# Optimization experiments

Hardware: AMD Instinct MI355X
Metric: run time of the kernel (lower is better)

The kernel has to match this reference:

```python
import jax, jax.numpy as jnp
import numpy as np

L = 16            # clip_len
STRIDES = (2, 2)
RADII = (0.15, 0.3)
NSAMPLES = (16, 32)
EPS = 1e-5
NEG_SLOPE = 0.2


def _fps(xyz, npoint):
    # furthest point sampling, xyz: (N, 3) -> (npoint,) int32 indices, start at 0
    N = xyz.shape[0]
    def step(carry, _):
        mind, last = carry
        d = jnp.sum((xyz - xyz[last]) ** 2, axis=-1)
        mind = jnp.minimum(mind, d)
        nxt = jnp.argmax(mind).astype(jnp.int32)
        return (mind, nxt), nxt
    _, rest = jax.lax.scan(step, (jnp.full((N,), 1e10, xyz.dtype), jnp.int32(0)), None, length=npoint - 1)
    return jnp.concatenate([jnp.zeros((1,), jnp.int32), rest])


def _shift_point(xyz, batch, N):
    # torch.roll(points, -1, dims=1) over the temporal axis, with last-frame extrapolation fix
    p = xyz.reshape(batch // L, L, N, 3)
    s = jnp.roll(p, -1, axis=1)
    shift_mean = jnp.mean(s[:, :-1] - p[:, :-1], axis=1)   # (Bc, N, 3)
    s = s.at[:, -1].set(p[:, -1] + shift_mean)
    return s.reshape(batch, N, 3)


def _conv_bn_lrelu(x, w, g, b):
    # 1x1 Conv2d (no bias) + GroupBN (per-channel over all other dims) + LeakyReLU(0.2)
    y = jnp.einsum('oc,bcnk->bonk', w, x)
    mu = jnp.mean(y, axis=(0, 2, 3), keepdims=True)
    var = jnp.var(y, axis=(0, 2, 3), keepdims=True)
    y = (y - mu) * jax.lax.rsqrt(var + EPS) * g[None, :, None, None] + b[None, :, None, None]
    return jnp.where(y > 0, y, NEG_SLOPE * y)


def _sa_module(xyz, features, stride, radius, nsample, layers):
    # xyz: (B, N, 3), features: (B, C, N)
    batch, N = xyz.shape[0], xyz.shape[1]
    q = _shift_point(xyz, batch, N)
    npoint = N // stride if stride > 1 else N
    if stride > 1:
        idx = jax.vmap(lambda p: _fps(p, npoint))(jax.lax.stop_gradient(q))  # (B, npoint)
        q = jax.vmap(lambda p, ix: p[ix])(q, idx)                            # (B, npoint, 3)
    # ball query: first `nsample` neighbors of each query within `radius`, padded with first hit
    d2 = jnp.sum((q[:, :, None, :] - xyz[:, None, :, :]) ** 2, axis=-1)      # (B, npoint, N)
    mask = d2 < radius * radius
    cand = jnp.where(mask, jnp.arange(N, dtype=jnp.int32)[None, None, :], N)
    srt = jnp.sort(cand, axis=-1)[..., :nsample]
    first = srt[..., :1]
    gidx = jnp.where(srt == N, first, srt)
    gidx = jnp.where(gidx == N, 0, gidx)                                     # fallback: no neighbor
    grouped_xyz = jax.vmap(lambda pts, ix: pts[ix])(xyz, gidx)               # (B, npoint, ns, 3)
    dp = (grouped_xyz - q[:, :, None, :]) / radius                           # normalize_dp
    dist = jnp.linalg.norm(dp, axis=-1)                                      # (B, npoint, ns) -> 4th grouped channel
    feats = jnp.swapaxes(features, 1, 2)                                     # (B, N, C)
    grouped_f = jax.vmap(lambda f, ix: f[ix])(feats, gidx)                   # (B, npoint, ns, C)
    x = jnp.concatenate([dp, grouped_f], axis=-1)                            # (B, npoint, ns, 3 + C)
    x = jnp.transpose(x, (0, 3, 1, 2))                                       # (B, 3 + C, npoint, ns)
    for (w, g, b) in layers:
        x = _conv_bn_lrelu(x, w, g, b)
    gate = jax.nn.sigmoid(dist)[:, None, :, :]                               # sigmoid(points[:, -1:])
    out = jnp.max(gate * x, axis=-1)                                         # (B, Cout, npoint)
    return q, out


def _forward(xyz, w1a, g1a, b1a, w1b, g1b, b1b, w2a, g2a, b2a, w2b, g2b, b2b):
    features = jnp.swapaxes(xyz, 1, 2)                                       # features default = xyz^T
    q1, f1 = _sa_module(xyz, features, STRIDES[0], RADII[0], NSAMPLES[0],
                        [(w1a, g1a, b1a), (w1b, g1b, b1b)])
    q2, f2 = _sa_module(q1, f1, STRIDES[1], RADII[1], NSAMPLES[1],
                        [(w2a, g2a, b2a), (w2b, g2b, b2b)])
    return f2                                                                # (32, 256, 128)


def setup_inputs() -> dict:
    key = jax.random.key(0)
    ks = jax.random.split(key, 5)
    B, N = 32, 512   # B = 2 clips * clip_len 16
    xyz = jax.random.uniform(ks[0], (B, N, 3), jnp.float32)
    def w(k, o, i):
        return jax.random.normal(k, (o, i), jnp.float32) / np.sqrt(i).astype(np.float32)
    return {
        'xyz': xyz,
        'w1a': w(ks[1], 64, 6),    'g1a': jnp.ones(64),  'b1a': jnp.zeros(64),
        'w1b': w(ks[2], 128, 64),  'g1b': jnp.ones(128), 'b1b': jnp.zeros(128),
        'w2a': w(ks[3], 128, 131), 'g2a': jnp.ones(128), 'b2a': jnp.zeros(128),
        'w2b': w(ks[4], 256, 128), 'g2b': jnp.ones(256), 'b2b': jnp.zeros(256),
    }


def reference(xyz, w1a, g1a, b1a, w1b, g1b, b1b, w2a, g2a, b2a, w2b, g2b, b2b):
    return _forward(xyz, w1a, g1a, b1a, w1b, g1b, b1b, w2a, g2a, b2a, w2b, g2b, b2b)
```

## Files before the change

kernel.cpp:

```cpp
#include <hip/hip_runtime.h>
#include <hip/hip_bf16.h>
#include <math.h>


#define BATCH 32
#define MCOLS 131072
#define CGRID 2048

typedef __attribute__((ext_vector_type(8))) short short8;
typedef __attribute__((ext_vector_type(4))) short short4v;
typedef __attribute__((ext_vector_type(4))) float f32x4;

__device__ __forceinline__ float b2f(short s) {
    return __uint_as_float(((unsigned)(unsigned short)s) << 16);
}
__device__ __forceinline__ short f2b(float f) {
    __hip_bfloat16 h = __float2bfloat16(f);
    return (short)__builtin_bit_cast(unsigned short, h);
}
__device__ __forceinline__ float dpp_row16_sum(float v) {
    int x;
    x = __builtin_amdgcn_update_dpp(0, __float_as_int(v), 0x111, 0xf, 0xf, true);
    v += __int_as_float(x);
    x = __builtin_amdgcn_update_dpp(0, __float_as_int(v), 0x112, 0xf, 0xf, true);
    v += __int_as_float(x);
    x = __builtin_amdgcn_update_dpp(0, __float_as_int(v), 0x114, 0xf, 0xf, true);
    v += __int_as_float(x);
    x = __builtin_amdgcn_update_dpp(0, __float_as_int(v), 0x118, 0xf, 0xf, true);
    v += __int_as_float(x);
    return v;
}
template<int C>
__device__ __forceinline__ float dpp_max(float v) {
    int x = __builtin_amdgcn_update_dpp(0, __float_as_int(v), C, 0xf, 0xf, true);
    return fmaxf(v, __int_as_float(x));
}
__device__ __forceinline__ float readlane_f(float v, int lane) {
    return __int_as_float(__builtin_amdgcn_readlane(__float_as_int(v), lane));
}

__global__ void prep_w(const float* __restrict__ w, int O, int C, int CK,
                       short* __restrict__ hi, short* __restrict__ lo) {
    int t = blockIdx.x * 256 + threadIdx.x;
    if (t >= O * CK) return;
    int o = t / CK, c = t % CK;
    float f = (c < C) ? w[o * C + c] : 0.f;
    short h = f2b(f);
    float fh = b2f(h);
    int NT = O >> 4;
    int ot = o >> 4, l15 = o & 15;
    int kc = c >> 5, quad = (c & 31) >> 3, j = c & 7;
    size_t idx = (((size_t)kc * NT + ot) * 64 + quad * 16 + l15) * 8 + j;
    hi[idx] = h;
    lo[idx] = f2b(f - fh);
}

template<int N, int NPOINT>
__global__ __launch_bounds__(64) void fps_kernel(const float* __restrict__ src,
                                                 float* __restrict__ qsel) {
    int b = blockIdx.x;
    int lane = threadIdx.x;
    int l = b & 15;
    constexpr int P = N / 64;
    __shared__ float4 qp[N];
    __shared__ int sel[NPOINT];
    if (l < 15) {
        const float* s = src + (size_t)(b + 1) * N * 3;
        for (int j = lane; j < N; j += 64)
            qp[j] = make_float4(s[j * 3 + 0], s[j * 3 + 1], s[j * 3 + 2], 0.f);
    } else {
        int g0 = b - 15;
        for (int j = lane; j < N; j += 64) {
            float v[3];
#pragma unroll
            for (int c = 0; c < 3; ++c) {
                float acc = 0.f;
                for (int i = 0; i < 15; ++i) {
                    float d = __fsub_rn(src[((size_t)(g0 + i + 1) * N + j) * 3 + c],
                                        src[((size_t)(g0 + i) * N + j) * 3 + c]);
                    acc = __fadd_rn(acc, d);
                }
                v[c] = __fadd_rn(src[((size_t)b * N + j) * 3 + c], __fdiv_rn(acc, 15.f));
            }
            qp[j] = make_float4(v[0], v[1], v[2], 0.f);
        }
    }
    if (lane == 0) sel[0] = 0;
    __syncthreads();
    float px[P], py[P], pz[P], mind[P];
#pragma unroll
    for (int p = 0; p < P; ++p) {
        float4 v = qp[lane * P + p];
        px[p] = v.x; py[p] = v.y; pz[p] = v.z;
        mind[p] = 1e10f;
    }
    float4 L0 = qp[0];
    float lx = L0.x, ly = L0.y, lz = L0.z;
    for (int s = 1; s < NPOINT; ++s) {
        float mn[P];
#pragma unroll
        for (int p = 0; p < P; ++p) {
            float dx = __fsub_rn(px[p], lx);
            float dy = __fsub_rn(py[p], ly);
            float dz = __fsub_rn(pz[p], lz);
            float d = __fadd_rn(__fadd_rn(__fmul_rn(dx, dx), __fmul_rn(dy, dy)),
                                __fmul_rn(dz, dz));
            float m2 = fminf(mind[p], d);
            mind[p] = m2;
            mn[p] = m2;
        }
        float t[P];
#pragma unroll
        for (int p = 0; p < P; ++p) t[p] = mn[p];
#pragma unroll
        for (int w = P / 2; w >= 1; w >>= 1)
#pragma unroll
            for (int p = 0; p < w; ++p) t[p] = fmaxf(t[p], t[p + w]);
        float local = t[0];
        float m = local;
        m = dpp_max<0x111>(m);
        m = dpp_max<0x112>(m);
        m = dpp_max<0x114>(m);
        m = dpp_max<0x118>(m);
        m = dpp_max<0x142>(m);
        m = dpp_max<0x143>(m);
        float maxd = readlane_f(m, 63);
        int enc = 0;
        float bx = px[0], by = py[0], bz = pz[0];
#pragma unroll
        for (int p = P - 1; p >= 1; --p) {
            bool e = (mn[p] == local);
            enc = e ? p : enc;
            bx = e ? px[p] : bx;
            by = e ? py[p] : by;
            bz = e ? pz[p] : bz;
        }
        bool e0 = (mn[0] == local);
        enc = e0 ? 0 : enc;
        bx = e0 ? px[0] : bx;
        by = e0 ? py[0] : by;
        bz = e0 ? pz[0] : bz;
        unsigned long long msk = __ballot(local == maxd);
        int winner = (int)__builtin_ctzll(msk);
        int last = winner * P + __builtin_amdgcn_readlane(enc, winner);
        lx = readlane_f(bx, winner);
        ly = readlane_f(by, winner);
        lz = readlane_f(bz, winner);
        if (lane == 0) sel[s] = last;
    }
    __syncthreads();
    for (int i = lane; i < NPOINT; i += 64) {
        float4 Pt = qp[sel[i]];
        size_t o = ((size_t)b * NPOINT + i) * 3;
        qsel[o + 0] = Pt.x;
        qsel[o + 1] = Pt.y;
        qsel[o + 2] = Pt.z;
    }
}

template<int N, int NPOINT, int NS, int CF, int CK>
__global__ __launch_bounds__(256) void ballq_kernel(
        const float* __restrict__ xyz,
        const float* __restrict__ qpts,
        const float* __restrict__ feats,
        float r2, float radius,
        short* __restrict__ X, float* __restrict__ gate) {
    static_assert((NS & (NS - 1)) == 0, "NS pow2");
    int lane = threadIdx.x & 63;
    int wib = threadIdx.x >> 6;
    int wid = blockIdx.x * 4 + wib;
    int b = wid / NPOINT;
    int i = wid % NPOINT;
    const float* qp = qpts + ((size_t)b * NPOINT + i) * 3;
    float qx = qp[0], qy = qp[1], qz = qp[2];
    __shared__ int gsh[4][NS];
    int* gidx = gsh[wib];
    int taken = 0, first = 0;
    bool any = false;
#pragma unroll
    for (int base = 0; base < N; base += 64) {
        int j = base + lane;
        const float* p = xyz + ((size_t)b * N + j) * 3;
        float dx = __fsub_rn(qx, p[0]);
        float dy = __fsub_rn(qy, p[1]);
        float dz = __fsub_rn(qz, p[2]);
        float d2 = __fadd_rn(__fadd_rn(__fmul_rn(dx, dx), __fmul_rn(dy, dy)),
                             __fmul_rn(dz, dz));
        bool in = d2 < r2;
        unsigned long long mk = __ballot(in);
        if (!any && mk) { first = base + __builtin_ctzll(mk); any = true; }
        int cb = __builtin_popcountll(mk & ((1ull << lane) - 1ull));
        int slot = taken + cb;
        if (in && slot < NS) gidx[slot] = j;
        taken += (int)__builtin_popcountll(mk);
    }
    if (taken < NS) {
        for (int s = taken + lane; s < NS; s += 64) gidx[s] = any ? first : 0;
    }
    __syncthreads();
    int m0 = (b * NPOINT + i) * NS;
    if (lane < NS) {
        int g = gidx[lane];
        const float* p = xyz + ((size_t)b * N + g) * 3;
        float dx = (p[0] - qx) / radius;
        float dy = (p[1] - qy) / radius;
        float dz = (p[2] - qz) / radius;
        float dist = sqrtf(dx * dx + dy * dy + dz * dz);
        gate[m0 + lane] = 1.f / (1.f + expf(-dist));
    }
    for (int e = lane; e < NS * CK; e += 64) {
        int s = e / CK;
        int c = e % CK;
        int g = gidx[s];
        float v;
        if (c < 3) {
            float qc = (c == 0) ? qx : ((c == 1) ? qy : qz);
            v = (xyz[((size_t)b * N + g) * 3 + c] - qc) / radius;
        } else if (c < 3 + CF) {
            v = feats[((size_t)b * N + g) * CF + (c - 3)];
        } else {
            v = 0.f;
        }
        X[(size_t)(m0 + s) * CK + c] = f2b(v);
    }
}

template<int CK, int O, bool AFF>
__global__ __launch_bounds__(256, 3) void mfma_conv(
        const short* __restrict__ X, const short* __restrict__ Whi,
        const short* __restrict__ Wlo, const float* __restrict__ ss,
        short* __restrict__ Y, float* __restrict__ pS, float* __restrict__ pS2) {
    constexpr int KC = CK / 32;
    constexpr int NT = O / 16;
    constexpr int OW = NT / 4;
    constexpr int LR = CK + 8;
    constexpr int CB = CK / 8;
    __shared__ __align__(16) short xs[64 * LR];
    __shared__ __align__(16) short wh[NT * 512];
    __shared__ __align__(16) short wl[NT * 512];
    __shared__ float ssl[AFF ? 2 * CK : 1];
    __shared__ float sblk[O], s2blk[O];
    int tid = threadIdx.x;
    int m0 = blockIdx.x * 64;

    if constexpr (AFF) {
        for (int i = tid; i < 2 * CK; i += 256) ssl[i] = ss[i];
        __syncthreads();
    }
    for (int idx = tid; idx < 64 * CB; idx += 256) {
        int r = idx / CB;
        int col = (idx % CB) * 8;
        short8 v = *(const short8*)(X + (size_t)(m0 + r) * CK + col);
        if constexpr (AFF) {
#pragma unroll
            for (int i = 0; i < 8; ++i) {
                float f = b2f(v[i]);
                f = fmaf(f, ssl[col + i], ssl[CK + col + i]);
                f = f > 0.f ? f : 0.2f * f;
                v[i] = f2b(f);
            }
        }
        *(short8*)(xs + r * LR + col) = v;
    }

    int lane = tid & 63;
    int wave = tid >> 6;
    int l15 = lane & 15;
    int quad = lane >> 4;
    int obase = wave * OW * 16;

    f32x4 acc[4][OW];
#pragma unroll
    for (int mt = 0; mt < 4; ++mt)
#pragma unroll
        for (int ot = 0; ot < OW; ++ot) acc[mt][ot] = (f32x4){0.f, 0.f, 0.f, 0.f};

    for (int kc = 0; kc < KC; ++kc) {
        __syncthreads();
        {
            const short8* gH = (const short8*)Whi + (size_t)kc * NT * 64;
            const short8* gL = (const short8*)Wlo + (size_t)kc * NT * 64;
            short8* lH = (short8*)wh;
            short8* lL = (short8*)wl;
            for (int i = tid; i < NT * 64; i += 256) { lH[i] = gH[i]; lL[i] = gL[i]; }
        }
        __syncthreads();
        short8 bf[4];
#pragma unroll
        for (int mt = 0; mt < 4; ++mt)
            bf[mt] = *(const short8*)(xs + (mt * 16 + l15) * LR + kc * 32 + quad * 8);
#pragma unroll
        for (int ot = 0; ot < OW; ++ot) {
            short8 ah = ((const short8*)wh)[(wave * OW + ot) * 64 + lane];
            short8 al = ((const short8*)wl)[(wave * OW + ot) * 64 + lane];
#pragma unroll
            for (int mt = 0; mt < 4; ++mt) {
                acc[mt][ot] = __builtin_amdgcn_mfma_f32_16x16x32_bf16(ah, bf[mt], acc[mt][ot], 0, 0, 0);
                acc[mt][ot] = __builtin_amdgcn_mfma_f32_16x16x32_bf16(al, bf[mt], acc[mt][ot], 0, 0, 0);
            }
        }
    }

#pragma unroll
    for (int mt = 0; mt < 4; ++mt) {
        size_t ybase = (size_t)(m0 + mt * 16 + l15) * O + obase + quad * 4;
#pragma unroll
        for (int ot = 0; ot < OW; ++ot) {
            short4v pk;
#pragma unroll
            for (int r4 = 0; r4 < 4; ++r4) pk[r4] = f2b(acc[mt][ot][r4]);
            *(short4v*)(Y + ybase + ot * 16) = pk;
        }
    }
#pragma unroll
    for (int ot = 0; ot < OW; ++ot) {
#pragma unroll
        for (int r4 = 0; r4 < 4; ++r4) {
            float s = 0.f, s2 = 0.f;
#pragma unroll
            for (int mt = 0; mt < 4; ++mt) {
                float v = acc[mt][ot][r4];
                s += v;
                s2 = fmaf(v, v, s2);
            }
            s = dpp_row16_sum(s);
            s2 = dpp_row16_sum(s2);
            if (l15 == 15) {
                int o = obase + ot * 16 + quad * 4 + r4;
                sblk[o] = s;
                s2blk[o] = s2;
            }
        }
    }
    __syncthreads();
    for (int o = tid; o < O; o += 256) {
        pS [(size_t)o * CGRID + blockIdx.x] = sblk[o];
        pS2[(size_t)o * CGRID + blockIdx.x] = s2blk[o];
    }
}

template<int O>
__global__ __launch_bounds__(256) void stats_fin(
        const float* __restrict__ pS, const float* __restrict__ pS2,
        const float* __restrict__ gm, const float* __restrict__ bt,
        float* __restrict__ norm) {
    int o = blockIdx.x;
    float s = 0.f, s2 = 0.f;
    for (int p = threadIdx.x; p < CGRID; p += 256) {
        s += pS[(size_t)o * CGRID + p];
        s2 += pS2[(size_t)o * CGRID + p];
    }
#pragma unroll
    for (int off = 32; off >= 1; off >>= 1) {
        s  += __shfl_xor(s,  off, 64);
        s2 += __shfl_xor(s2, off, 64);
    }
    __shared__ float sh[8];
    int wid = threadIdx.x >> 6;
    if ((threadIdx.x & 63) == 0) { sh[wid] = s; sh[4 + wid] = s2; }
    __syncthreads();
    if (threadIdx.x == 0) {
        float S  = sh[0] + sh[1] + sh[2] + sh[3];
        float S2 = sh[4] + sh[5] + sh[6] + sh[7];
        const float invM = 1.f / (float)MCOLS;
        float mu = S * invM;
        float var = S2 * invM - mu * mu;
        float sc = gm[o] * rsqrtf(var + 1e-5f);
        norm[o] = sc;
        norm[O + o] = bt[o] - mu * sc;
    }
}

template<int NS, int NPOINT, int O>
__global__ __launch_bounds__(256) void pool1_kernel(
        const short* __restrict__ Y, const float* __restrict__ norm,
        const float* __restrict__ gate, float* __restrict__ out) {
    int t = blockIdx.x * 256 + threadIdx.x;
    int o = t % O;
    int n = (t / O) % NPOINT;
    int b = t / (O * NPOINT);
    int m0 = (b * NPOINT + n) * NS;
    float sc = norm[o], sf = norm[O + o];
    float best = -INFINITY;
#pragma unroll
    for (int k = 0; k < NS; ++k) {
        float v = fmaf(b2f(Y[(size_t)(m0 + k) * O + o]), sc, sf);
        v = v > 0.f ? v : 0.2f * v;
        best = fmaxf(best, gate[m0 + k] * v);
    }
    out[t] = best;
}

__global__ __launch_bounds__(256) void pool2_kernel(
        const short* __restrict__ Y, const float* __restrict__ norm,
        const float* __restrict__ gate, float* __restrict__ out) {
    constexpr int NS = 32, NPOINT = 128, O = 256;
    int b  = blockIdx.x >> 3;
    int oc = (blockIdx.x >> 1) & 3;
    int nc = blockIdx.x & 1;
    __shared__ float trans[64][65];
    int tid = threadIdx.x;
    for (int w = 0; w < 16; ++w) {
        int idx = w * 256 + tid;
        int o_l = idx & 63;
        int n_l = idx >> 6;
        int o = oc * 64 + o_l;
        int n = nc * 64 + n_l;
        int m0 = (b * NPOINT + n) * NS;
        float sc = norm[o], sf = norm[O + o];
        float best = -INFINITY;
#pragma unroll
        for (int k = 0; k < NS; ++k) {
            float v = fmaf(b2f(Y[(size_t)(m0 + k) * O + o]), sc, sf);
            v = v > 0.f ? v : 0.2f * v;
            best = fmaxf(best, gate[m0 + k] * v);
        }
        trans[o_l][n_l] = best;
    }
    __syncthreads();
    for (int w = 0; w < 16; ++w) {
        int idx = w * 256 + tid;
        int o_l = idx >> 6;
        int n_l = idx & 63;
        out[((size_t)b * O + oc * 64 + o_l) * NPOINT + nc * 64 + n_l] = trans[o_l][n_l];
    }
}

extern "C" void kernel_launch(void* const* d_in, const int* in_sizes, int n_in,
                              void* d_out, int out_size, void* d_ws, size_t ws_size,
                              hipStream_t stream) {
    const float* xyz = (const float*)d_in[0];
    const float* w1a = (const float*)d_in[1];
    const float* g1a = (const float*)d_in[2];
    const float* b1a = (const float*)d_in[3];
    const float* w1b = (const float*)d_in[4];
    const float* g1b = (const float*)d_in[5];
    const float* b1b = (const float*)d_in[6];
    const float* w2a = (const float*)d_in[7];
    const float* g2a = (const float*)d_in[8];
    const float* b2a = (const float*)d_in[9];
    const float* w2b = (const float*)d_in[10];
    const float* g2b = (const float*)d_in[11];
    const float* b2b = (const float*)d_in[12];

    char* ws = (char*)d_ws;
    constexpr size_t OFF_Q1C   = 0;
    constexpr size_t OFF_GATE1 = 98304;
    constexpr size_t OFF_Q2C   = 622592;
    constexpr size_t OFF_GATE2 = 671744;
    constexpr size_t OFF_NORM  = 1196032;
    constexpr size_t OFF_W     = 1204224;
    constexpr size_t OFF_PS    = 1499136;
    constexpr size_t OFF_PS2   = 3596288;
    constexpr size_t OFF_A     = 5693440;
    constexpr size_t OFF_B     = 39247872;
    constexpr size_t OFF_F1    = OFF_B + 41943040;

    float* q1c   = (float*)(ws + OFF_Q1C);
    float* gate1 = (float*)(ws + OFF_GATE1);
    float* q2c   = (float*)(ws + OFF_Q2C);
    float* gate2 = (float*)(ws + OFF_GATE2);
    float* n1a   = (float*)(ws + OFF_NORM);
    float* n1b   = (float*)(ws + OFF_NORM + 512);
    float* n2a   = (float*)(ws + OFF_NORM + 1536);
    float* n2b   = (float*)(ws + OFF_NORM + 2560);
    short* w1aH  = (short*)(ws + OFF_W);
    short* w1aL  = w1aH + 2048;
    short* w1bH  = w1aL + 2048;
    short* w1bL  = w1bH + 8192;
    short* w2aH  = w1bL + 8192;
    short* w2aL  = w2aH + 20480;
    short* w2bH  = w2aL + 20480;
    short* w2bL  = w2bH + 32768;
    float* pS    = (float*)(ws + OFF_PS);
    float* pS2   = (float*)(ws + OFF_PS2);

    char* A = ws + OFF_A;
    char* B = ws + OFF_B;
    short* X1  = (short*)A;
    short* Y1a = (short*)B;
    short* Y1b = (short*)A;
    short* X2  = (short*)B;
    short* Y2a = (short*)A;
    short* Y2b = (short*)B;
    float* f1  = (float*)(ws + OFF_F1);

    const float r2_1 = (float)(0.15 * 0.15);
    const float r2_2 = (float)(0.3 * 0.3);

    prep_w<<<8,   256, 0, stream>>>(w1a, 64, 6, 32, w1aH, w1aL);
    prep_w<<<32,  256, 0, stream>>>(w1b, 128, 64, 64, w1bH, w1bL);
    prep_w<<<80,  256, 0, stream>>>(w2a, 128, 131, 160, w2aH, w2aL);
    prep_w<<<128, 256, 0, stream>>>(w2b, 256, 128, 128, w2bH, w2bL);

    fps_kernel<512, 256><<<32, 64, 0, stream>>>(xyz, q1c);
    ballq_kernel<512, 256, 16, 3, 32><<<2048, 256, 0, stream>>>(
        xyz, q1c, xyz, r2_1, 0.15f, X1, gate1);
    mfma_conv<32, 64, false><<<CGRID, 256, 0, stream>>>(X1, w1aH, w1aL, nullptr, Y1a, pS, pS2);
    stats_fin<64><<<64, 256, 0, stream>>>(pS, pS2, g1a, b1a, n1a);
    mfma_conv<64, 128, true><<<CGRID, 256, 0, stream>>>(Y1a, w1bH, w1bL, n1a, Y1b, pS, pS2);
    stats_fin<128><<<128, 256, 0, stream>>>(pS, pS2, g1b, b1b, n1b);
    pool1_kernel<16, 256, 128><<<4096, 256, 0, stream>>>(Y1b, n1b, gate1, f1);

    fps_kernel<256, 128><<<32, 64, 0, stream>>>(q1c, q2c);
    ballq_kernel<256, 128, 32, 128, 160><<<1024, 256, 0, stream>>>(
        q1c, q2c, f1, r2_2, 0.3f, X2, gate2);
    mfma_conv<160, 128, false><<<CGRID, 256, 0, stream>>>(X2, w2aH, w2aL, nullptr, Y2a, pS, pS2);
    stats_fin<128><<<128, 256, 0, stream>>>(pS, pS2, g2a, b2a, n2a);
    mfma_conv<128, 256, true><<<CGRID, 256, 0, stream>>>(Y2a, w2bH, w2bL, n2a, Y2b, pS, pS2);
    stats_fin<256><<<256, 256, 0, stream>>>(pS, pS2, g2b, b2b, n2b);
    pool2_kernel<<<256, 256, 0, stream>>>(Y2b, n2b, gate2, (float*)d_out);
}
```

Baseline: 434.3 us.

## Fuse setup kernels, atomic BN stats, drop stats_fin, parallelize shift, vectorize stores

Merges the four weight-prep launches and the temporal shift into one setup kernel, moving the shift out of the serial FPS kernel into fully parallel per-element work. BatchNorm partial sums are now accumulated with atomics into a small zeroed buffer, and the scale/shift is recomputed inside consumer kernels, so the separate stats_fin launches go away. Conv outputs are staged through LDS for coalesced 16-byte stores, and ball-query gather writes eight bf16 values at once. Atomic float accumulation makes the statistics order-nondeterministic and adds contention on a few addresses.

```diff
diff --git a/kernel.cpp b/kernel.cpp
--- a/kernel.cpp
+++ b/kernel.cpp
@@ -39,9 +39,9 @@
     return __int_as_float(__builtin_amdgcn_readlane(__float_as_int(v), lane));
 }
 
-__global__ void prep_w(const float* __restrict__ w, int O, int C, int CK,
-                       short* __restrict__ hi, short* __restrict__ lo) {
-    int t = blockIdx.x * 256 + threadIdx.x;
+__device__ __forceinline__ void prep_elem(const float* __restrict__ w, int O, int C,
+                                          int CK, short* __restrict__ hi,
+                                          short* __restrict__ lo, int t) {
     if (t >= O * CK) return;
     int o = t / CK, c = t % CK;
     float f = (c < C) ? w[o * C + c] : 0.f;
@@ -55,36 +55,57 @@
     lo[idx] = f2b(f - fh);
 }
 
+__device__ __forceinline__ void shift_elem(const float* __restrict__ xyz,
+                                           float* __restrict__ qout, int t, int N) {
+    int c = t % 3;
+    int n = (t / 3) % N;
+    int b = t / (3 * N);
+    int l = b & 15;
+    float v;
+    if (l < 15) {
+        v = xyz[((size_t)(b + 1) * N + n) * 3 + c];
+    } else {
+        int g0 = b - 15;
+        float acc = 0.f;
+        for (int i = 0; i < 15; ++i) {
+            float d = __fsub_rn(xyz[((size_t)(g0 + i + 1) * N + n) * 3 + c],
+                                xyz[((size_t)(g0 + i) * N + n) * 3 + c]);
+            acc = __fadd_rn(acc, d);
+        }
+        v = __fadd_rn(xyz[((size_t)b * N + n) * 3 + c], __fdiv_rn(acc, 15.f));
+    }
+    qout[t] = v;
+}
+
+__global__ __launch_bounds__(256) void setup_kernel(
+        const float* __restrict__ w1a, const float* __restrict__ w1b,
+        const float* __restrict__ w2a, const float* __restrict__ w2b,
+        const float* __restrict__ xyz, float* __restrict__ qs1,
+        short* w1aH, short* w1aL, short* w1bH, short* w1bL,
+        short* w2aH, short* w2aL, short* w2bH, short* w2bL) {
+    int bid = blockIdx.x;
+    int tid = threadIdx.x;
+    if (bid < 8)        prep_elem(w1a, 64, 6, 32,    w1aH, w1aL, bid * 256 + tid);
+    else if (bid < 40)  prep_elem(w1b, 128, 64, 64,  w1bH, w1bL, (bid - 8) * 256 + tid);
+    else if (bid < 120) prep_elem(w2a, 128, 131, 160, w2aH, w2aL, (bid - 40) * 256 + tid);
+    else if (bid < 248) prep_elem(w2b, 256, 128, 128, w2bH, w2bL, (bid - 120) * 256 + tid);
+    else {
+        int t = (bid - 248) * 256 + tid;
+        if (t < BATCH * 512 * 3) shift_elem(xyz, qs1, t, 512);
+    }
+}
+
 template<int N, int NPOINT>
-__global__ __launch_bounds__(64) void fps_kernel(const float* __restrict__ src,
+__global__ __launch_bounds__(64) void fps_kernel(const float* __restrict__ q,
                                                  float* __restrict__ qsel) {
     int b = blockIdx.x;
     int lane = threadIdx.x;
-    int l = b & 15;
     constexpr int P = N / 64;
     __shared__ float4 qp[N];
     __shared__ int sel[NPOINT];
-    if (l < 15) {
-        const float* s = src + (size_t)(b + 1) * N * 3;
-        for (int j = lane; j < N; j += 64)
-            qp[j] = make_float4(s[j * 3 + 0], s[j * 3 + 1], s[j * 3 + 2], 0.f);
-    } else {
-        int g0 = b - 15;
-        for (int j = lane; j < N; j += 64) {
-            float v[3];
-#pragma unroll
-            for (int c = 0; c < 3; ++c) {
-                float acc = 0.f;
-                for (int i = 0; i < 15; ++i) {
-                    float d = __fsub_rn(src[((size_t)(g0 + i + 1) * N + j) * 3 + c],
-                                        src[((size_t)(g0 + i) * N + j) * 3 + c]);
-                    acc = __fadd_rn(acc, d);
-                }
-                v[c] = __fadd_rn(src[((size_t)b * N + j) * 3 + c], __fdiv_rn(acc, 15.f));
-            }
-            qp[j] = make_float4(v[0], v[1], v[2], 0.f);
-        }
-    }
+    const float* qb = q + (size_t)b * N * 3;
+    for (int j = lane; j < N; j += 64)
+        qp[j] = make_float4(qb[j * 3 + 0], qb[j * 3 + 1], qb[j * 3 + 2], 0.f);
     if (lane == 0) sel[0] = 0;
     __syncthreads();
     float px[P], py[P], pz[P], mind[P];
@@ -125,21 +146,16 @@
         m = dpp_max<0x142>(m);
         m = dpp_max<0x143>(m);
         float maxd = readlane_f(m, 63);
-        int enc = 0;
-        float bx = px[0], by = py[0], bz = pz[0];
-#pragma unroll
-        for (int p = P - 1; p >= 1; --p) {
+        int enc = P - 1;
+        float bx = px[P - 1], by = py[P - 1], bz = pz[P - 1];
+#pragma unroll
+        for (int p = P - 2; p >= 0; --p) {
             bool e = (mn[p] == local);
             enc = e ? p : enc;
             bx = e ? px[p] : bx;
             by = e ? py[p] : by;
             bz = e ? pz[p] : bz;
         }
-        bool e0 = (mn[0] == local);
-        enc = e0 ? 0 : enc;
-        bx = e0 ? px[0] : bx;
-        by = e0 ? py[0] : by;
-        bz = e0 ? pz[0] : bz;
         unsigned long long msk = __ballot(local == maxd);
         int winner = (int)__builtin_ctzll(msk);
         int last = winner * P + __builtin_amdgcn_readlane(enc, winner);
@@ -166,6 +182,7 @@
         float r2, float radius,
         short* __restrict__ X, float* __restrict__ gate) {
     static_assert((NS & (NS - 1)) == 0, "NS pow2");
+    static_assert(CK % 8 == 0, "CK mult of 8");
     int lane = threadIdx.x & 63;
     int wib = threadIdx.x >> 6;
     int wid = blockIdx.x * 4 + wib;
@@ -208,43 +225,64 @@
         float dist = sqrtf(dx * dx + dy * dy + dz * dz);
         gate[m0 + lane] = 1.f / (1.f + expf(-dist));
     }
-    for (int e = lane; e < NS * CK; e += 64) {
-        int s = e / CK;
-        int c = e % CK;
+    for (int e8 = lane * 8; e8 < NS * CK; e8 += 64 * 8) {
+        int s = e8 / CK;
+        int c0 = e8 % CK;
         int g = gidx[s];
-        float v;
-        if (c < 3) {
-            float qc = (c == 0) ? qx : ((c == 1) ? qy : qz);
-            v = (xyz[((size_t)b * N + g) * 3 + c] - qc) / radius;
-        } else if (c < 3 + CF) {
-            v = feats[((size_t)b * N + g) * CF + (c - 3)];
-        } else {
-            v = 0.f;
-        }
-        X[(size_t)(m0 + s) * CK + c] = f2b(v);
+        const float* frow = feats + (size_t)(b * N + g) * CF;
+        const float* prow = xyz + ((size_t)b * N + g) * 3;
+        short8 v8;
+#pragma unroll
+        for (int ii = 0; ii < 8; ++ii) {
+            int c = c0 + ii;
+            float v;
+            if (c < 3) {
+                float qc = (c == 0) ? qx : ((c == 1) ? qy : qz);
+                v = (prow[c] - qc) / radius;
+            } else if (c < 3 + CF) {
+                v = frow[c - 3];
+            } else {
+                v = 0.f;
+            }
+            v8[ii] = f2b(v);
+        }
+        *(short8*)(X + (size_t)(m0 + s) * CK + c0) = v8;
     }
 }
 
 template<int CK, int O, bool AFF>
 __global__ __launch_bounds__(256, 3) void mfma_conv(
         const short* __restrict__ X, const short* __restrict__ Whi,
-        const short* __restrict__ Wlo, const float* __restrict__ ss,
-        short* __restrict__ Y, float* __restrict__ pS, float* __restrict__ pS2) {
+        const short* __restrict__ Wlo,
+        const float* __restrict__ aS,
+        const float* __restrict__ gm, const float* __restrict__ bt,
+        float* __restrict__ mySums,
+        short* __restrict__ Y) {
     constexpr int KC = CK / 32;
     constexpr int NT = O / 16;
     constexpr int OW = NT / 4;
     constexpr int LR = CK + 8;
+    constexpr int LRY = O + 10;
     constexpr int CB = CK / 8;
-    __shared__ __align__(16) short xs[64 * LR];
+    constexpr int XSZ = (64 * LR > 32 * LRY) ? 64 * LR : 32 * LRY;
+    __shared__ __align__(16) short xsbuf[XSZ];
     __shared__ __align__(16) short wh[NT * 512];
     __shared__ __align__(16) short wl[NT * 512];
-    __shared__ float ssl[AFF ? 2 * CK : 1];
-    __shared__ float sblk[O], s2blk[O];
+    __shared__ float ssl[AFF ? 2 * CK : 2];
     int tid = threadIdx.x;
     int m0 = blockIdx.x * 64;
+    short* xs = xsbuf;
 
     if constexpr (AFF) {
-        for (int i = tid; i < 2 * CK; i += 256) ssl[i] = ss[i];
+        const float invM = 1.f / (float)MCOLS;
+        for (int i = tid; i < CK; i += 256) {
+            float S = aS[i], S2 = aS[CK + i];
+            float mu = S * invM;
+            float var = S2 * invM - mu * mu;
+            float sc = gm[i] * rsqrtf(var + 1e-5f);
+            ssl[i] = sc;
+            ssl[CK + i] = bt[i] - mu * sc;
+        }
         __syncthreads();
     }
     for (int idx = tid; idx < 64 * CB; idx += 256) {
@@ -301,17 +339,6 @@
         }
     }
 
-#pragma unroll
-    for (int mt = 0; mt < 4; ++mt) {
-        size_t ybase = (size_t)(m0 + mt * 16 + l15) * O + obase + quad * 4;
-#pragma unroll
-        for (int ot = 0; ot < OW; ++ot) {
-            short4v pk;
-#pragma unroll
-            for (int r4 = 0; r4 < 4; ++r4) pk[r4] = f2b(acc[mt][ot][r4]);
-            *(short4v*)(Y + ybase + ot * 16) = pk;
-        }
-    }
 #pragma unroll
     for (int ot = 0; ot < OW; ++ot) {
 #pragma unroll
@@ -327,60 +354,60 @@
             s2 = dpp_row16_sum(s2);
             if (l15 == 15) {
                 int o = obase + ot * 16 + quad * 4 + r4;
-                sblk[o] = s;
-                s2blk[o] = s2;
+                atomicAdd(&mySums[o], s);
+                atomicAdd(&mySums[O + o], s2);
             }
         }
     }
-    __syncthreads();
-    for (int o = tid; o < O; o += 256) {
-        pS [(size_t)o * CGRID + blockIdx.x] = sblk[o];
-        pS2[(size_t)o * CGRID + blockIdx.x] = s2blk[o];
-    }
-}
-
-template<int O>
-__global__ __launch_bounds__(256) void stats_fin(
-        const float* __restrict__ pS, const float* __restrict__ pS2,
+
+    short* ys = xsbuf;
+    for (int half = 0; half < 2; ++half) {
+        __syncthreads();
+#pragma unroll
+        for (int mh = 0; mh < 2; ++mh) {
+            int mt = half * 2 + mh;
+            int r = mh * 16 + l15;
+#pragma unroll
+            for (int ot = 0; ot < OW; ++ot) {
+                short4v pk;
+#pragma unroll
+                for (int r4 = 0; r4 < 4; ++r4) pk[r4] = f2b(acc[mt][ot][r4]);
+                *(short4v*)(ys + r * LRY + obase + ot * 16 + quad * 4) = pk;
+            }
+        }
+        __syncthreads();
+        constexpr int CHUNKS = 32 * O / 8;
+        for (int i = tid; i < CHUNKS; i += 256) {
+            int r = i / (O / 8);
+            int col = (i % (O / 8)) * 8;
+            *(short8*)(Y + (size_t)(m0 + half * 32 + r) * O + col) =
+                *(const short8*)(ys + r * LRY + col);
+        }
+    }
+}
+
+__global__ __launch_bounds__(256) void pool1_shift2_kernel(
+        const short* __restrict__ Y, const float* __restrict__ aS,
         const float* __restrict__ gm, const float* __restrict__ bt,
-        float* __restrict__ norm) {
-    int o = blockIdx.x;
-    float s = 0.f, s2 = 0.f;
-    for (int p = threadIdx.x; p < CGRID; p += 256) {
-        s += pS[(size_t)o * CGRID + p];
-        s2 += pS2[(size_t)o * CGRID + p];
-    }
-#pragma unroll
-    for (int off = 32; off >= 1; off >>= 1) {
-        s  += __shfl_xor(s,  off, 64);
-        s2 += __shfl_xor(s2, off, 64);
-    }
-    __shared__ float sh[8];
-    int wid = threadIdx.x >> 6;
-    if ((threadIdx.x & 63) == 0) { sh[wid] = s; sh[4 + wid] = s2; }
-    __syncthreads();
-    if (threadIdx.x == 0) {
-        float S  = sh[0] + sh[1] + sh[2] + sh[3];
-        float S2 = sh[4] + sh[5] + sh[6] + sh[7];
-        const float invM = 1.f / (float)MCOLS;
-        float mu = S * invM;
-        float var = S2 * invM - mu * mu;
-        float sc = gm[o] * rsqrtf(var + 1e-5f);
-        norm[o] = sc;
-        norm[O + o] = bt[o] - mu * sc;
-    }
-}
-
-template<int NS, int NPOINT, int O>
-__global__ __launch_bounds__(256) void pool1_kernel(
-        const short* __restrict__ Y, const float* __restrict__ norm,
-        const float* __restrict__ gate, float* __restrict__ out) {
+        const float* __restrict__ gate, float* __restrict__ out,
+        const float* __restrict__ q1c, float* __restrict__ qs2) {
+    constexpr int NS = 16, NPOINT = 256, O = 128;
+    if (blockIdx.x >= 4096) {
+        int t = (int)(blockIdx.x - 4096) * 256 + threadIdx.x;
+        if (t < BATCH * 256 * 3) shift_elem(q1c, qs2, t, 256);
+        return;
+    }
     int t = blockIdx.x * 256 + threadIdx.x;
     int o = t % O;
     int n = (t / O) % NPOINT;
     int b = t / (O * NPOINT);
     int m0 = (b * NPOINT + n) * NS;
-    float sc = norm[o], sf = norm[O + o];
+    const float invM = 1.f / (float)MCOLS;
+    float S = aS[o], S2 = aS[O + o];
+    float mu = S * invM;
+    float var = S2 * invM - mu * mu;
+    float sc = gm[o] * rsqrtf(var + 1e-5f);
+    float sf = bt[o] - mu * sc;
     float best = -INFINITY;
 #pragma unroll
     for (int k = 0; k < NS; ++k) {
@@ -392,14 +419,27 @@
 }
 
 __global__ __launch_bounds__(256) void pool2_kernel(
-        const short* __restrict__ Y, const float* __restrict__ norm,
+        const short* __restrict__ Y, const float* __restrict__ aS,
+        const float* __restrict__ gm, const float* __restrict__ bt,
         const float* __restrict__ gate, float* __restrict__ out) {
     constexpr int NS = 32, NPOINT = 128, O = 256;
     int b  = blockIdx.x >> 3;
     int oc = (blockIdx.x >> 1) & 3;
     int nc = blockIdx.x & 1;
     __shared__ float trans[64][65];
+    __shared__ float sscale[64], sshift[64];
     int tid = threadIdx.x;
+    if (tid < 64) {
+        int o = oc * 64 + tid;
+        const float invM = 1.f / (float)MCOLS;
+        float S = aS[o], S2 = aS[O + o];
+        float mu = S * invM;
+        float var = S2 * invM - mu * mu;
+        float sc = gm[o] * rsqrtf(var + 1e-5f);
+        sscale[tid] = sc;
+        sshift[tid] = bt[o] - mu * sc;
+    }
+    __syncthreads();
     for (int w = 0; w < 16; ++w) {
         int idx = w * 256 + tid;
         int o_l = idx & 63;
@@ -407,7 +447,7 @@
         int o = oc * 64 + o_l;
         int n = nc * 64 + n_l;
         int m0 = (b * NPOINT + n) * NS;
-        float sc = norm[o], sf = norm[O + o];
+        float sc = sscale[o_l], sf = sshift[o_l];
         float best = -INFINITY;
 #pragma unroll
         for (int k = 0; k < NS; ++k) {
@@ -448,10 +488,8 @@
     constexpr size_t OFF_GATE1 = 98304;
     constexpr size_t OFF_Q2C   = 622592;
     constexpr size_t OFF_GATE2 = 671744;
-    constexpr size_t OFF_NORM  = 1196032;
     constexpr size_t OFF_W     = 1204224;
-    constexpr size_t OFF_PS    = 1499136;
-    constexpr size_t OFF_PS2   = 3596288;
+    constexpr size_t OFF_SUMS  = 1499136;
     constexpr size_t OFF_A     = 5693440;
     constexpr size_t OFF_B     = 39247872;
     constexpr size_t OFF_F1    = OFF_B + 41943040;
@@ -460,10 +498,6 @@
     float* gate1 = (float*)(ws + OFF_GATE1);
     float* q2c   = (float*)(ws + OFF_Q2C);
     float* gate2 = (float*)(ws + OFF_GATE2);
-    float* n1a   = (float*)(ws + OFF_NORM);
-    float* n1b   = (float*)(ws + OFF_NORM + 512);
-    float* n2a   = (float*)(ws + OFF_NORM + 1536);
-    float* n2b   = (float*)(ws + OFF_NORM + 2560);
     short* w1aH  = (short*)(ws + OFF_W);
     short* w1aL  = w1aH + 2048;
     short* w1bH  = w1aL + 2048;
@@ -472,8 +506,11 @@
     short* w2aL  = w2aH + 20480;
     short* w2bH  = w2aL + 20480;
     short* w2bL  = w2bH + 32768;
-    float* pS    = (float*)(ws + OFF_PS);
-    float* pS2   = (float*)(ws + OFF_PS2);
+    float* sums  = (float*)(ws + OFF_SUMS);
+    float* s1a   = sums;
+    float* s1b   = sums + 128;
+    float* s2a   = sums + 384;
+    float* s2b   = sums + 640;
 
     char* A = ws + OFF_A;
     char* B = ws + OFF_B;
@@ -483,31 +520,34 @@
     short* X2  = (short*)B;
     short* Y2a = (short*)A;
     short* Y2b = (short*)B;
+    float* qs1 = (float*)B;
+    float* qs2 = (float*)A;
     float* f1  = (float*)(ws + OFF_F1);
 
     const float r2_1 = (float)(0.15 * 0.15);
     const float r2_2 = (float)(0.3 * 0.3);
 
-    prep_w<<<8,   256, 0, stream>>>(w1a, 64, 6, 32, w1aH, w1aL);
-    prep_w<<<32,  256, 0, stream>>>(w1b, 128, 64, 64, w1bH, w1bL);
-    prep_w<<<80,  256, 0, stream>>>(w2a, 128, 131, 160, w2aH, w2aL);
-    prep_w<<<128, 256, 0, stream>>>(w2b, 256, 128, 128, w2bH, w2bL);
-
-    fps_kernel<512, 256><<<32, 64, 0, stream>>>(xyz, q1c);
+    hipMemsetAsync(sums, 0, 1152 * sizeof(float), stream);
+    setup_kernel<<<440, 256, 0, stream>>>(w1a, w1b, w2a, w2b, xyz, qs1,
+                                          w1aH, w1aL, w1bH, w1bL,
+                                          w2aH, w2aL, w2bH, w2bL);
+
+    fps_kernel<512, 256><<<32, 64, 0, stream>>>(qs1, q1c);
     ballq_kernel<512, 256, 16, 3, 32><<<2048, 256, 0, stream>>>(
         xyz, q1c, xyz, r2_1, 0.15f, X1, gate1);
-    mfma_conv<32, 64, false><<<CGRID, 256, 0, stream>>>(X1, w1aH, w1aL, nullptr, Y1a, pS, pS2);
-    stats_fin<64><<<64, 256, 0, stream>>>(pS, pS2, g1a, b1a, n1a);
-    mfma_conv<64, 128, true><<<CGRID, 256, 0, stream>>>(Y1a, w1bH, w1bL, n1a, Y1b, pS, pS2);
-    stats_fin<128><<<128, 256, 0, stream>>>(pS, pS2, g1b, b1b, n1b);
-    pool1_kernel<16, 256, 128><<<4096, 256, 0, stream>>>(Y1b, n1b, gate1, f1);
-
-    fps_kernel<256, 128><<<32, 64, 0, stream>>>(q1c, q2c);
+    mfma_conv<32, 64, false><<<CGRID, 256, 0, stream>>>(
+        X1, w1aH, w1aL, nullptr, nullptr, nullptr, s1a, Y1a);
+    mfma_conv<64, 128, true><<<CGRID, 256, 0, stream>>>(
+        Y1a, w1bH, w1bL, s1a, g1a, b1a, s1b, Y1b);
+    pool1_shift2_kernel<<<4192, 256, 0, stream>>>(
+        Y1b, s1b, g1b, b1b, gate1, f1, q1c, qs2);
+
+    fps_kernel<256, 128><<<32, 64, 0, stream>>>(qs2, q2c);
     ballq_kernel<256, 128, 32, 128, 160><<<1024, 256, 0, stream>>>(
         q1c, q2c, f1, r2_2, 0.3f, X2, gate2);
-    mfma_conv<160, 128, false><<<CGRID, 256, 0, stream>>>(X2, w2aH, w2aL, nullptr, Y2a, pS, pS2);
-    stats_fin<128><<<128, 256, 0, stream>>>(pS, pS2, g2a, b2a, n2a);
-    mfma_conv<128, 256, true><<<CGRID, 256, 0, stream>>>(Y2a, w2bH, w2bL, n2a, Y2b, pS, pS2);
-    stats_fin<256><<<256, 256, 0, stream>>>(pS, pS2, g2b, b2b, n2b);
-    pool2_kernel<<<256, 256, 0, stream>>>(Y2b, n2b, gate2, (float*)d_out);
-}
+    mfma_conv<160, 128, false><<<CGRID, 256, 0, stream>>>(
+        X2, w2aH, w2aL, nullptr, nullptr, nullptr, s2a, Y2a);
+    mfma_conv<128, 256, true><<<CGRID, 256, 0, stream>>>(
+        Y2a, w2bH, w2bL, s2a, g2a, b2a, s2b, Y2b);
+    pool2_kernel<<<256, 256, 0, stream>>>(Y2b, s2b, g2b, b2b, gate2, (float*)d_out);
+}
```

New measurement: 1.105 ms. 2.54x slower.
